# Performance work log

Hardware: AMD Instinct MI355X
Metric: run time of the kernel (lower is better)

## Reference

```python
import jax, jax.numpy as jnp
import numpy as np

H = 8
D_MODEL = 1024
D_K = D_MODEL // H
NEG = -1000000000.0


def layer_norm(x, a, b, eps=1e-06):
    # torch std: unbiased (ddof=1); module divides by (std + eps)
    mean = jnp.mean(x, axis=-1, keepdims=True)
    var = jnp.sum((x - mean) ** 2, axis=-1, keepdims=True) / (x.shape[-1] - 1)
    std = jnp.sqrt(var)
    return a * (x - mean) / (std + eps) + b


def setup_inputs() -> dict:
    key = jax.random.key(0)
    ks = jax.random.split(key, 12)
    B, S, D = 8, 1024, D_MODEL
    inp = {
        "query": jax.random.normal(ks[0], (B, S, D), jnp.float32),
        "value": jax.random.normal(ks[1], (B, S, D), jnp.float32),
        "key": jax.random.normal(ks[2], (B, S, D), jnp.float32),
        "mask": jax.random.randint(ks[3], (B, S), 0, 2, jnp.int32),
        "ln_a": jnp.ones((D,), jnp.float32),
        "ln_b": jnp.zeros((D,), jnp.float32),
        "wq": jax.random.normal(ks[4], (D, D), jnp.float32) * 0.02,
        "bq": jnp.zeros((D,), jnp.float32),
        "wk": jax.random.normal(ks[5], (D, D), jnp.float32) * 0.02,
        "bk": jnp.zeros((D,), jnp.float32),
        "wv": jax.random.normal(ks[6], (D, D), jnp.float32) * 0.02,
        "bv": jnp.zeros((D,), jnp.float32),
        "w_aoa": jax.random.normal(ks[7], (2 * D, 2 * D), jnp.float32) * 0.02,  # [out, in]
        "b_aoa": jnp.zeros((2 * D,), jnp.float32),
    }
    return inp


def reference(query, value, key, mask, ln_a, ln_b, wq, bq, wk, bk, wv, bv, w_aoa, b_aoa):
    B, S, D = query.shape
    # mask [B,S] -> [B,1,1,S]
    m = mask[:, None, None, :]
    # norm_q
    q = layer_norm(query, ln_a, ln_b)
    # QKV projections, split heads -> [B,H,S,Dk]
    def split_heads(x):
        return x.reshape(B, -1, H, D_K).transpose(0, 2, 1, 3)
    q_ = split_heads(q @ wq.T + bq)
    k_ = split_heads(key @ wk.T + bk)
    v_ = split_heads(value @ wv.T + bv)
    scores = jnp.einsum("bhqd,bhkd->bhqk", q_, k_) / jnp.sqrt(jnp.float32(D_K))
    scores = jnp.where(m == 0, NEG, scores)
    p = jax.nn.softmax(scores, axis=-1)
    x = jnp.einsum("bhqk,bhkd->bhqd", p, v_)
    x = x.transpose(0, 2, 1, 3).reshape(B, S, D)
    # AoA: concat with (normed) query, linear to 2D, GLU
    z = jnp.concatenate([x, q], axis=-1) @ w_aoa.T + b_aoa
    a, g = jnp.split(z, 2, axis=-1)
    return a * jax.nn.sigmoid(g)
```

## Files before the change

kernel.cpp:

```cpp
#include <hip/hip_runtime.h>

typedef __attribute__((ext_vector_type(8))) __bf16 bf16x8;
typedef __attribute__((ext_vector_type(4))) float f32x4;
typedef __attribute__((ext_vector_type(16))) float f32x16;

__device__ __forceinline__ ushort f2b(float f) {
    uint u = __builtin_bit_cast(uint, f);
    u += 0x7fffu + ((u >> 16) & 1u);
    return (ushort)(u >> 16);
}
__device__ __forceinline__ float b2f(ushort h) {
    uint u = ((uint)h) << 16;
    return __builtin_bit_cast(float, u);
}

__global__ __launch_bounds__(256) void cast_kernel(const float* __restrict__ src,
                                                   ushort* __restrict__ dst) {
    size_t i = ((size_t)blockIdx.x * 256 + threadIdx.x) * 4;
    float4 v = *(const float4*)(src + i);
    ushort4 o;
    o.x = f2b(v.x); o.y = f2b(v.y); o.z = f2b(v.z); o.w = f2b(v.w);
    *(ushort4*)(dst + i) = o;
}

__global__ __launch_bounds__(256) void cast_permute_aoa(const float* __restrict__ src,
                                                        ushort* __restrict__ dst) {
    int n1 = blockIdx.x >> 1;
    int c = (blockIdx.x & 1) * 1024 + threadIdx.x * 4;
    int q = ((n1 & 63) | ((n1 >> 7) << 6)) + ((n1 >> 6) & 1) * 1024;
    float4 v = *(const float4*)(src + (size_t)q * 2048 + c);
    ushort4 o;
    o.x = f2b(v.x); o.y = f2b(v.y); o.z = f2b(v.z); o.w = f2b(v.w);
    *(ushort4*)(dst + (size_t)n1 * 2048 + c) = o;
}

__global__ __launch_bounds__(256) void ln_kernel(const float* __restrict__ x,
                                                 const float* __restrict__ ga,
                                                 const float* __restrict__ be,
                                                 ushort* __restrict__ xq) {
    const int row = blockIdx.x, tid = threadIdx.x;
    __shared__ float red[4];
    float4 v = ((const float4*)(x + (size_t)row * 1024))[tid];
    float sm = v.x + v.y + v.z + v.w;
    for (int off = 32; off; off >>= 1) sm += __shfl_xor(sm, off);
    if ((tid & 63) == 0) red[tid >> 6] = sm;
    __syncthreads();
    float mean = (red[0] + red[1] + red[2] + red[3]) * (1.f / 1024.f);
    __syncthreads();
    float dx = v.x - mean, dy = v.y - mean, dz = v.z - mean, dw = v.w - mean;
    float s2 = dx * dx + dy * dy + dz * dz + dw * dw;
    for (int off = 32; off; off >>= 1) s2 += __shfl_xor(s2, off);
    if ((tid & 63) == 0) red[tid >> 6] = s2;
    __syncthreads();
    float var = (red[0] + red[1] + red[2] + red[3]) * (1.f / 1023.f);
    float inv = 1.f / (sqrtf(var) + 1e-6f);
    float4 g = ((const float4*)ga)[tid];
    float4 bb = ((const float4*)be)[tid];
    ushort4 o;
    o.x = f2b(g.x * dx * inv + bb.x);
    o.y = f2b(g.y * dy * inv + bb.y);
    o.z = f2b(g.z * dz * inv + bb.z);
    o.w = f2b(g.w * dw * inv + bb.w);
    *(ushort4*)&xq[(size_t)row * 2048 + 1024 + tid * 4] = o;
}

template <int MODE>
__global__ __launch_bounds__(512, 2) void gemm6(const ushort* __restrict__ Aq, int ldaq,
                                                const ushort* __restrict__ Ak,
                                                const ushort* __restrict__ Av,
                                                const ushort* __restrict__ B, int ldb,
                                                const float* __restrict__ bias0,
                                                const float* __restrict__ bias1,
                                                const float* __restrict__ bias2,
                                                void* __restrict__ out0,
                                                void* __restrict__ out1,
                                                void* __restrict__ out2,
                                                int K, int NB, float qscale) {
    __shared__ ushort lds[2][32768];

    const int tid = threadIdx.x;
    const int w = tid >> 6, l = tid & 63;
    const int wr = w >> 2, wcn = w & 3;
    const int r16 = l & 15, g4 = l >> 4;

    const int bid = blockIdx.x;
    const int cpx = gridDim.x >> 3;
    const int swz = (bid & 7) * cpx + (bid >> 3);
    const int m0 = (swz / NB) * 256;
    const int n0 = (swz % NB) * 256;

    const int region = (MODE == 0) ? (n0 >> 10) : 0;
    const ushort* A = (MODE == 0) ? (region == 0 ? Aq : (region == 1 ? Ak : Av)) : Aq;
    const int lda = (MODE == 0) ? (region == 0 ? ldaq : 1024) : ldaq;

    const int srow8 = l >> 3;
    const int sxor8 = ((l & 7) ^ srow8) * 8;
    const ushort* As0 = A + (size_t)(m0 + w * 8 + srow8) * lda + sxor8;
    const ushort* Bs0 = B + (size_t)(n0 + w * 8 + srow8) * ldb + sxor8;

    f32x4 acc[8][4];
#pragma unroll
    for (int i = 0; i < 8; i++)
#pragma unroll
        for (int j = 0; j < 4; j++) acc[i][j] = (f32x4){0.f, 0.f, 0.f, 0.f};

    const int sw16 = (r16 & 7) << 4;
    char* ldsb = (char*)&lds[0][0];

#define STAGE_H(sel_, HS_, kt_)                                                            \
    do {                                                                                   \
        const int mat_ = (HS_)&1, half_ = (HS_) >> 1;                                      \
        const ushort* sb_ = mat_ ? Bs0 : As0;                                              \
        const int ld_ = mat_ ? ldb : lda;                                                  \
        _Pragma("unroll") for (int li_ = 0; li_ < 2; li_++) {                              \
            const ushort* src_ = sb_ + (size_t)(half_ * 128 + li_ * 64) * ld_ + (kt_)*64;  \
            int dst_ = (sel_)*65536 + mat_ * 32768 + half_ * 16384 + li_ * 8192 + w * 1024;\
            __builtin_amdgcn_global_load_lds(                                              \
                (const __attribute__((address_space(1))) void*)src_,                       \
                (__attribute__((address_space(3))) void*)(ldsb + dst_), 16, 0, 0);         \
        }                                                                                  \
    } while (0)

    auto LDA4 = [&](bf16x8 (&dst)[4][2], int sel, int half) {
#pragma unroll
        for (int ai = 0; ai < 4; ai++)
#pragma unroll
            for (int ks = 0; ks < 2; ks++)
                dst[ai][ks] = *(const bf16x8*)(ldsb + sel * 65536 + half * 16384 +
                                               (wr * 16 + 32 * ai + r16) * 128 +
                                               ((ks * 64 + g4 * 16) ^ sw16));
    };
    auto LDB2 = [&](bf16x8 (&dst)[2][2], int sel, int half) {
#pragma unroll
        for (int bi = 0; bi < 2; bi++)
#pragma unroll
            for (int ks = 0; ks < 2; ks++)
                dst[bi][ks] = *(const bf16x8*)(ldsb + sel * 65536 + 32768 + half * 16384 +
                                               (wcn * 16 + 64 * bi + r16) * 128 +
                                               ((ks * 64 + g4 * 16) ^ sw16));
    };
    auto MM = [&](bf16x8 (&af)[4][2], bf16x8 (&bf)[2][2], int A0, int B0) {
        __builtin_amdgcn_s_setprio(1);
#pragma unroll
        for (int ks = 0; ks < 2; ks++)
#pragma unroll
            for (int ai = 0; ai < 4; ai++)
#pragma unroll
                for (int bi = 0; bi < 2; bi++)
                    acc[A0 + ai][B0 + bi] = __builtin_amdgcn_mfma_f32_16x16x32_bf16(
                        af[ai][ks], bf[bi][ks], acc[A0 + ai][B0 + bi], 0, 0, 0);
        __builtin_amdgcn_s_setprio(0);
    };

    const int NT = K >> 6;

    STAGE_H(0, 0, 0); STAGE_H(0, 1, 0); STAGE_H(0, 2, 0); STAGE_H(0, 3, 0);
    STAGE_H(1, 0, 1); STAGE_H(1, 1, 1); STAGE_H(1, 2, 1);
    asm volatile("s_waitcnt vmcnt(10)" ::: "memory");
    __builtin_amdgcn_s_barrier();

    bf16x8 aL[4][2], aH[4][2], bL[2][2], bH[2][2];

    for (int t = 0; t < NT - 2; ++t) {
        const int sel = t & 1;
        LDA4(aL, sel, 0); LDB2(bL, sel, 0);
        STAGE_H(sel ^ 1, 3, t + 1);
        __builtin_amdgcn_s_barrier();
        MM(aL, bL, 0, 0);
        asm volatile("s_waitcnt vmcnt(10)" ::: "memory");
        __builtin_amdgcn_s_barrier();
        LDA4(aH, sel, 1);
        STAGE_H(sel, 0, t + 2);
        __builtin_amdgcn_s_barrier();
        MM(aH, bL, 4, 0);
        asm volatile("s_waitcnt vmcnt(10)" ::: "memory");
        __builtin_amdgcn_s_barrier();
        LDB2(bH, sel, 1);
        STAGE_H(sel, 1, t + 2);
        __builtin_amdgcn_s_barrier();
        MM(aH, bH, 4, 2);
        __builtin_amdgcn_s_barrier();
        STAGE_H(sel, 2, t + 2);
        __builtin_amdgcn_s_barrier();
        MM(aL, bH, 0, 2);
        asm volatile("s_waitcnt vmcnt(10)" ::: "memory");
        __builtin_amdgcn_s_barrier();
    }
    {
        const int sel = (NT - 2) & 1;
        LDA4(aL, sel, 0); LDB2(bL, sel, 0);
        STAGE_H(sel ^ 1, 3, NT - 1);
        __builtin_amdgcn_s_barrier();
        MM(aL, bL, 0, 0);
        asm volatile("s_waitcnt vmcnt(10)" ::: "memory");
        __builtin_amdgcn_s_barrier();
        LDA4(aH, sel, 1);
        __builtin_amdgcn_s_barrier();
        MM(aH, bL, 4, 0);
        asm volatile("s_waitcnt vmcnt(8)" ::: "memory");
        __builtin_amdgcn_s_barrier();
        LDB2(bH, sel, 1);
        __builtin_amdgcn_s_barrier();
        MM(aH, bH, 4, 2);
        __builtin_amdgcn_s_barrier();
        MM(aL, bH, 0, 2);
        asm volatile("s_waitcnt vmcnt(4)" ::: "memory");
        __builtin_amdgcn_s_barrier();
    }
    {
        const int sel = (NT - 1) & 1;
        LDA4(aL, sel, 0); LDB2(bL, sel, 0);
        __builtin_amdgcn_s_barrier();
        MM(aL, bL, 0, 0);
        asm volatile("s_waitcnt vmcnt(2)" ::: "memory");
        __builtin_amdgcn_s_barrier();
        LDA4(aH, sel, 1);
        __builtin_amdgcn_s_barrier();
        MM(aH, bL, 4, 0);
        asm volatile("s_waitcnt vmcnt(0)" ::: "memory");
        __builtin_amdgcn_s_barrier();
        LDB2(bH, sel, 1);
        MM(aH, bH, 4, 2);
        MM(aL, bH, 0, 2);
    }
#undef STAGE_H

    if (MODE == 1) {
        float* out = (float*)out0;
#pragma unroll
        for (int bp = 0; bp < 2; bp++) {
            int j = (n0 >> 1) + wcn * 16 + 64 * bp + r16;
            float bsa = bias0[j];
            float bsg = bias0[j + 1024];
#pragma unroll
            for (int a_ = 0; a_ < 8; a_++) {
                int mr = m0 + wr * 16 + 32 * a_ + g4 * 4;
#pragma unroll
                for (int r = 0; r < 4; r++) {
                    float av = acc[a_][2 * bp][r] + bsa;
                    float gv = acc[a_][2 * bp + 1][r] + bsg;
                    out[(size_t)(mr + r) * 1024 + j] = av * (1.f / (1.f + __expf(-gv)));
                }
            }
        }
    } else {
        const int nr0 = n0 & 1023;
        const float* bias = region == 0 ? bias0 : (region == 1 ? bias1 : bias2);
        const float scale = region == 0 ? qscale : 1.f;
        if (region < 2) {
            ushort* C = (ushort*)(region == 0 ? out0 : out1);
#pragma unroll
            for (int b_ = 0; b_ < 4; b_++) {
                int n = nr0 + wcn * 16 + 64 * b_ + r16;
                float bs = bias[n];
#pragma unroll
                for (int a_ = 0; a_ < 8; a_++) {
                    int mr = m0 + wr * 16 + 32 * a_ + g4 * 4;
#pragma unroll
                    for (int r = 0; r < 4; r++)
                        C[(size_t)(mr + r) * 1024 + n] = f2b((acc[a_][b_][r] + bs) * scale);
                }
            }
        } else {
            ushort* Vt = (ushort*)out2;
#pragma unroll
            for (int b_ = 0; b_ < 4; b_++) {
                int n = nr0 + wcn * 16 + 64 * b_ + r16;
                float bs = bias[n];
                int h = n >> 7, d = n & 127;
#pragma unroll
                for (int a_ = 0; a_ < 8; a_++) {
                    int mr = m0 + wr * 16 + 32 * a_ + g4 * 4;
                    int bb = mr >> 10, s_ = mr & 1023;
                    ushort4 o;
                    o.x = f2b(acc[a_][b_][0] + bs);
                    o.y = f2b(acc[a_][b_][1] + bs);
                    o.z = f2b(acc[a_][b_][2] + bs);
                    o.w = f2b(acc[a_][b_][3] + bs);
                    *(ushort4*)&Vt[((size_t)(bb * 8 + h) * 128 + d) * 1024 + s_] = o;
                }
            }
        }
    }
}

__global__ __launch_bounds__(512, 2) void attn_kernel(const ushort* __restrict__ Q,
                                                      const ushort* __restrict__ Kt,
                                                      const ushort* __restrict__ Vt,
                                                      const int* __restrict__ mask,
                                                      ushort* __restrict__ xq) {
    __shared__ ushort Ks[2][8192];
    __shared__ ushort Vs[2][8192];
    __shared__ ushort Pl[8][2048];

    const int tid = threadIdx.x;
    const int l = tid & 63, wid = tid >> 6;
    const int ql = l & 31, hi = l >> 5;
    const int id = blockIdx.x;
    const int bh = ((id >> 5) << 3) | (id & 7);
    const int qb = (id >> 3) & 3;
    const int b = bh >> 3, h = bh & 7;
    const int q0 = qb * 256 + wid * 32;

    bf16x8 qf[8];
    const ushort* Qrow = Q + (size_t)(b * 1024 + q0 + ql) * 1024 + h * 128 + hi * 8;
#pragma unroll
    for (int ks = 0; ks < 8; ks++) qf[ks] = *(const bf16x8*)(Qrow + ks * 16);

    const ushort* Kg = Kt + ((size_t)b * 1024) * 1024 + h * 128;
    const ushort* Vg = Vt + (size_t)(b * 8 + h) * 128 * 1024;
    const int* mptr = mask + b * 1024;

    f32x16 xacc[4];
#pragma unroll
    for (int i = 0; i < 4; i++)
#pragma unroll
        for (int r = 0; r < 16; r++) xacc[i][r] = 0.f;
    float mrow = -INFINITY, lrow = 0.f, sclp = 0.f;

    char* Pme = (char*)&Pl[wid][0];
    const int pswz = (ql & 7) << 4;

    auto STAGE_K = [&](int sel, int t) {
        const int kv0 = t * 64;
#pragma unroll
        for (int it = 0; it < 2; ++it) {
            int ob = it * 8192 + wid * 1024;
            int o = ob + l * 16;
            int row = o >> 8;
            int sc = (o & 255) ^ ((row & 7) << 4);
            const ushort* src = Kg + (size_t)(kv0 + row) * 1024 + (sc >> 1);
            __builtin_amdgcn_global_load_lds((const __attribute__((address_space(1))) void*)src,
                (__attribute__((address_space(3))) void*)((char*)&Ks[sel][0] + ob), 16, 0, 0);
        }
    };
    auto STAGE_V = [&](int sel, int t) {
        const int kv0 = t * 64;
#pragma unroll
        for (int it = 0; it < 2; ++it) {
            int ob = it * 8192 + wid * 1024;
            int o = ob + l * 16;
            int d = o >> 7;
            int sc = (o & 127) ^ ((d & 7) << 4);
            const ushort* src = Vg + (size_t)d * 1024 + kv0 + (sc >> 1);
            __builtin_amdgcn_global_load_lds((const __attribute__((address_space(1))) void*)src,
                (__attribute__((address_space(3))) void*)((char*)&Vs[sel][0] + ob), 16, 0, 0);
        }
    };

    auto QK = [&](f32x16 (&s)[2], int sel, unsigned long long wt) {
        const char* Kb_ = (const char*)&Ks[sel][0];
#pragma unroll
        for (int sub = 0; sub < 2; sub++) {
            f32x16 sacc;
#pragma unroll
            for (int r = 0; r < 16; r++) sacc[r] = 0.f;
            const int rowk = sub * 32 + ql;
            const char* kr = Kb_ + rowk * 256;
            const int sw = (rowk & 7) << 4;
            __builtin_amdgcn_s_setprio(1);
#pragma unroll
            for (int ks = 0; ks < 8; ks++) {
                bf16x8 kfr = *(const bf16x8*)(kr + ((ks * 32 + hi * 16) ^ sw));
                sacc = __builtin_amdgcn_mfma_f32_32x32x16_bf16(kfr, qf[ks], sacc, 0, 0, 0);
            }
            __builtin_amdgcn_s_setprio(0);
#pragma unroll
            for (int q2 = 0; q2 < 4; q2++) {
                uint nib = (uint)(wt >> (8 * q2 + 4 * hi + 32 * sub)) & 15u;
#pragma unroll
                for (int r = 0; r < 4; r++)
                    if (!((nib >> r) & 1u)) sacc[4 * q2 + r] = -1e9f;
            }
            s[sub] = sacc;
        }
    };
    auto PV = [&](int sel) {
        const char* Vb_ = (const char*)&Vs[sel][0];
        const int vsw = (ql & 7) << 4;
#pragma unroll
        for (int df = 0; df < 4; df++)
#pragma unroll
            for (int r = 0; r < 16; r++) xacc[df][r] *= sclp;
#pragma unroll
        for (int ks2 = 0; ks2 < 4; ks2++) {
            bf16x8 pfr = *(const bf16x8*)(Pme + ql * 128 + ((ks2 * 32 + hi * 16) ^ pswz));
            __builtin_amdgcn_s_setprio(1);
#pragma unroll
            for (int df = 0; df < 4; df++) {
                const int d = df * 32 + ql;
                bf16x8 vfr = *(const bf16x8*)(Vb_ + d * 128 + ((ks2 * 32 + hi * 16) ^ vsw));
                xacc[df] = __builtin_amdgcn_mfma_f32_32x32x16_bf16(vfr, pfr, xacc[df], 0, 0, 0);
            }
            __builtin_amdgcn_s_setprio(0);
        }
    };
    auto SOFTMAX = [&](f32x16 (&s)[2]) {
        float pmax = -INFINITY;
#pragma unroll
        for (int res = 0; res < 2; res++)
#pragma unroll
            for (int r = 0; r < 16; r++) pmax = fmaxf(pmax, s[res][r]);
        pmax = fmaxf(pmax, __shfl_xor(pmax, 32));
        float mn = fmaxf(mrow, pmax);
        sclp = __expf(mrow - mn);
        mrow = mn;
        float rsum = 0.f;
#pragma unroll
        for (int res = 0; res < 2; res++)
#pragma unroll
            for (int r = 0; r < 16; r++) {
                float p = __expf(s[res][r] - mn);
                s[res][r] = p;
                rsum += p;
            }
        rsum += __shfl_xor(rsum, 32);
        lrow = lrow * sclp + rsum;
#pragma unroll
        for (int res = 0; res < 2; res++)
#pragma unroll
            for (int q2 = 0; q2 < 4; q2++) {
                uint lo = ((uint)f2b(s[res][4 * q2 + 1]) << 16) | f2b(s[res][4 * q2]);
                uint hi2 = ((uint)f2b(s[res][4 * q2 + 3]) << 16) | f2b(s[res][4 * q2 + 2]);
                uint2 pk; pk.x = lo; pk.y = hi2;
                *(uint2*)(Pme + ql * 128 + ((16 * q2 + 8 * hi + 64 * res) ^ pswz)) = pk;
            }
    };

    STAGE_K(0, 0);
    int mv = mptr[l];
    asm volatile("s_waitcnt vmcnt(0)" ::: "memory");
    __syncthreads();
    STAGE_K(1, 1);
    STAGE_V(0, 0);
    unsigned long long wt = __ballot(mv != 0);
    mv = mptr[64 + l];
    f32x16 s[2];
    QK(s, 0, wt);
    SOFTMAX(s);
    int kc = 1, vc = 0;

    for (int u = 1; u < 16; ++u) {
        wt = __ballot(mv != 0);
        asm volatile("s_waitcnt vmcnt(0)" ::: "memory");
        __syncthreads();
        if (u < 15) STAGE_K(kc ^ 1, u + 1);
        STAGE_V(vc ^ 1, u);
        if (u < 15) mv = mptr[(u + 1) * 64 + l];

        QK(s, kc, wt);
        PV(vc);
        SOFTMAX(s);

        kc ^= 1; vc ^= 1;
    }

    asm volatile("s_waitcnt vmcnt(0)" ::: "memory");
    __syncthreads();
    PV(vc);

    const float inv = 1.f / lrow;
    const size_t orow = (size_t)(b * 1024 + q0 + ql) * 2048 + h * 128;
#pragma unroll
    for (int df = 0; df < 4; df++) {
#pragma unroll
        for (int q2 = 0; q2 < 4; q2++) {
            ushort4 o;
            o.x = f2b(xacc[df][4 * q2 + 0] * inv);
            o.y = f2b(xacc[df][4 * q2 + 1] * inv);
            o.z = f2b(xacc[df][4 * q2 + 2] * inv);
            o.w = f2b(xacc[df][4 * q2 + 3] * inv);
            *(ushort4*)&xq[orow + df * 32 + 8 * q2 + 4 * hi] = o;
        }
    }
}

extern "C" void kernel_launch(void* const* d_in, const int* in_sizes, int n_in,
                              void* d_out, int out_size, void* d_ws, size_t ws_size,
                              hipStream_t stream) {
    const float* query = (const float*)d_in[0];
    const float* value = (const float*)d_in[1];
    const float* key   = (const float*)d_in[2];
    const int*   mask  = (const int*)d_in[3];
    const float* ln_a  = (const float*)d_in[4];
    const float* ln_b  = (const float*)d_in[5];
    const float* wq    = (const float*)d_in[6];
    const float* bq    = (const float*)d_in[7];
    const float* wk    = (const float*)d_in[8];
    const float* bk    = (const float*)d_in[9];
    const float* wv    = (const float*)d_in[10];
    const float* bv    = (const float*)d_in[11];
    const float* waoa  = (const float*)d_in[12];
    const float* baoa  = (const float*)d_in[13];
    float* out = (float*)d_out;

    char* w8 = (char*)d_ws;
    ushort* xq   = (ushort*)(w8);
    ushort* Qb   = (ushort*)(w8 + 33554432);
    ushort* Kb   = (ushort*)(w8 + 50331648);
    ushort* Vt   = (ushort*)(w8 + 67108864);
    ushort* keyb = (ushort*)(w8 + 83886080);
    ushort* valb = (ushort*)(w8 + 100663296);
    ushort* wqb  = (ushort*)(w8 + 117440512);
    ushort* wkb  = (ushort*)(w8 + 119537664);
    ushort* wvb  = (ushort*)(w8 + 121634816);
    ushort* wab  = (ushort*)(w8 + 123731968);

    cast_kernel<<<8192, 256, 0, stream>>>(key, keyb);
    cast_kernel<<<8192, 256, 0, stream>>>(value, valb);
    cast_kernel<<<1024, 256, 0, stream>>>(wq, wqb);
    cast_kernel<<<1024, 256, 0, stream>>>(wk, wkb);
    cast_kernel<<<1024, 256, 0, stream>>>(wv, wvb);
    cast_permute_aoa<<<4096, 256, 0, stream>>>(waoa, wab);
    ln_kernel<<<8192, 256, 0, stream>>>(query, ln_a, ln_b, xq);

    const float qscale = 0.08838834764831845f;

    gemm6<0><<<384, 512, 0, stream>>>(xq + 1024, 2048, keyb, valb,
                                      wqb, 1024, bq, bk, bv,
                                      Qb, Kb, Vt, 1024, 12, qscale);

    attn_kernel<<<256, 512, 0, stream>>>(Qb, Kb, Vt, mask, xq);

    gemm6<1><<<256, 512, 0, stream>>>(xq, 2048, nullptr, nullptr,
                                      wab, 2048, baoa, nullptr, nullptr,
                                      out, nullptr, nullptr, 2048, 8, 1.f);
}
```

Before: 239.5 us.

## Keep softmax probabilities in registers via permlane32 swap and shrink attention blocks

The P tile no longer round-trips through LDS. Probabilities are packed with v_cvt_pk_bf16_f32 and rearranged across half-waves with permlane32_swap so they can feed the PV MFMA directly as operands. The attention block shrinks from 8 waves to 4, with 512 blocks each handling 128 queries and the K/V staging loops adjusted to match. This saves LDS traffic and LDS space for P but doubles the K/V tile loads per query, since fewer waves share each staged tile.

```diff
diff --git a/kernel.cpp b/kernel.cpp
--- a/kernel.cpp
+++ b/kernel.cpp
@@ -3,6 +3,7 @@
 typedef __attribute__((ext_vector_type(8))) __bf16 bf16x8;
 typedef __attribute__((ext_vector_type(4))) float f32x4;
 typedef __attribute__((ext_vector_type(16))) float f32x16;
+typedef __attribute__((ext_vector_type(2))) int i32x2;
 
 __device__ __forceinline__ ushort f2b(float f) {
     uint u = __builtin_bit_cast(uint, f);
@@ -12,6 +13,11 @@
 __device__ __forceinline__ float b2f(ushort h) {
     uint u = ((uint)h) << 16;
     return __builtin_bit_cast(float, u);
+}
+__device__ __forceinline__ uint cvtpk(float a, float b) {
+    uint r;
+    asm("v_cvt_pk_bf16_f32 %0, %1, %2" : "=v"(r) : "v"(a), "v"(b));
+    return r;
 }
 
 __global__ __launch_bounds__(256) void cast_kernel(const float* __restrict__ src,
@@ -284,23 +290,22 @@
     }
 }
 
-__global__ __launch_bounds__(512, 2) void attn_kernel(const ushort* __restrict__ Q,
+__global__ __launch_bounds__(256, 2) void attn_kernel(const ushort* __restrict__ Q,
                                                       const ushort* __restrict__ Kt,
                                                       const ushort* __restrict__ Vt,
                                                       const int* __restrict__ mask,
                                                       ushort* __restrict__ xq) {
     __shared__ ushort Ks[2][8192];
     __shared__ ushort Vs[2][8192];
-    __shared__ ushort Pl[8][2048];
 
     const int tid = threadIdx.x;
     const int l = tid & 63, wid = tid >> 6;
     const int ql = l & 31, hi = l >> 5;
     const int id = blockIdx.x;
-    const int bh = ((id >> 5) << 3) | (id & 7);
-    const int qb = (id >> 3) & 3;
+    const int bh = ((id >> 6) << 3) | (id & 7);
+    const int qb = (id >> 3) & 7;
     const int b = bh >> 3, h = bh & 7;
-    const int q0 = qb * 256 + wid * 32;
+    const int q0 = qb * 128 + wid * 32;
 
     bf16x8 qf[8];
     const ushort* Qrow = Q + (size_t)(b * 1024 + q0 + ql) * 1024 + h * 128 + hi * 8;
@@ -317,15 +322,13 @@
 #pragma unroll
         for (int r = 0; r < 16; r++) xacc[i][r] = 0.f;
     float mrow = -INFINITY, lrow = 0.f, sclp = 0.f;
-
-    char* Pme = (char*)&Pl[wid][0];
-    const int pswz = (ql & 7) << 4;
+    bf16x8 pa[4];
 
     auto STAGE_K = [&](int sel, int t) {
         const int kv0 = t * 64;
 #pragma unroll
-        for (int it = 0; it < 2; ++it) {
-            int ob = it * 8192 + wid * 1024;
+        for (int it = 0; it < 4; ++it) {
+            int ob = it * 4096 + wid * 1024;
             int o = ob + l * 16;
             int row = o >> 8;
             int sc = (o & 255) ^ ((row & 7) << 4);
@@ -337,8 +340,8 @@
     auto STAGE_V = [&](int sel, int t) {
         const int kv0 = t * 64;
 #pragma unroll
-        for (int it = 0; it < 2; ++it) {
-            int ob = it * 8192 + wid * 1024;
+        for (int it = 0; it < 4; ++it) {
+            int ob = it * 4096 + wid * 1024;
             int o = ob + l * 16;
             int d = o >> 7;
             int sc = (o & 127) ^ ((d & 7) << 4);
@@ -377,23 +380,21 @@
     };
     auto PV = [&](int sel) {
         const char* Vb_ = (const char*)&Vs[sel][0];
-        const int vsw = (ql & 7) << 4;
 #pragma unroll
         for (int df = 0; df < 4; df++)
 #pragma unroll
             for (int r = 0; r < 16; r++) xacc[df][r] *= sclp;
+        __builtin_amdgcn_s_setprio(1);
 #pragma unroll
         for (int ks2 = 0; ks2 < 4; ks2++) {
-            bf16x8 pfr = *(const bf16x8*)(Pme + ql * 128 + ((ks2 * 32 + hi * 16) ^ pswz));
-            __builtin_amdgcn_s_setprio(1);
 #pragma unroll
             for (int df = 0; df < 4; df++) {
                 const int d = df * 32 + ql;
-                bf16x8 vfr = *(const bf16x8*)(Vb_ + d * 128 + ((ks2 * 32 + hi * 16) ^ vsw));
-                xacc[df] = __builtin_amdgcn_mfma_f32_32x32x16_bf16(vfr, pfr, xacc[df], 0, 0, 0);
-            }
-            __builtin_amdgcn_s_setprio(0);
-        }
+                bf16x8 vfr = *(const bf16x8*)(Vb_ + d * 128 + ((ks2 * 32 + hi * 16) ^ ((d & 7) << 4)));
+                xacc[df] = __builtin_amdgcn_mfma_f32_32x32x16_bf16(vfr, pa[ks2], xacc[df], 0, 0, 0);
+            }
+        }
+        __builtin_amdgcn_s_setprio(0);
     };
     auto SOFTMAX = [&](f32x16 (&s)[2]) {
         float pmax = -INFINITY;
@@ -417,13 +418,22 @@
         rsum += __shfl_xor(rsum, 32);
         lrow = lrow * sclp + rsum;
 #pragma unroll
-        for (int res = 0; res < 2; res++)
-#pragma unroll
-            for (int q2 = 0; q2 < 4; q2++) {
-                uint lo = ((uint)f2b(s[res][4 * q2 + 1]) << 16) | f2b(s[res][4 * q2]);
-                uint hi2 = ((uint)f2b(s[res][4 * q2 + 3]) << 16) | f2b(s[res][4 * q2 + 2]);
-                uint2 pk; pk.x = lo; pk.y = hi2;
-                *(uint2*)(Pme + ql * 128 + ((16 * q2 + 8 * hi + 64 * res) ^ pswz)) = pk;
+        for (int sub = 0; sub < 2; sub++)
+#pragma unroll
+            for (int g = 0; g < 2; g++) {
+                const int b0 = g * 8;
+                uint lo01 = cvtpk(s[sub][b0 + 0], s[sub][b0 + 1]);
+                uint lo23 = cvtpk(s[sub][b0 + 2], s[sub][b0 + 3]);
+                uint hi01 = cvtpk(s[sub][b0 + 4], s[sub][b0 + 5]);
+                uint hi23 = cvtpk(s[sub][b0 + 6], s[sub][b0 + 7]);
+                i32x2 r02 = __builtin_amdgcn_permlane32_swap((int)lo01, (int)hi01, false, false);
+                i32x2 r13 = __builtin_amdgcn_permlane32_swap((int)lo23, (int)hi23, false, false);
+                union { bf16x8 v; uint u[4]; } pk;
+                pk.u[0] = (uint)r02.x;
+                pk.u[1] = (uint)r13.x;
+                pk.u[2] = (uint)r02.y;
+                pk.u[3] = (uint)r13.y;
+                pa[sub * 2 + g] = pk.v;
             }
     };
 
@@ -520,7 +530,7 @@
                                       wqb, 1024, bq, bk, bv,
                                       Qb, Kb, Vt, 1024, 12, qscale);
 
-    attn_kernel<<<256, 512, 0, stream>>>(Qb, Kb, Vt, mask, xq);
+    attn_kernel<<<512, 256, 0, stream>>>(Qb, Kb, Vt, mask, xq);
 
     gemm6<1><<<256, 512, 0, stream>>>(xq, 2048, nullptr, nullptr,
                                       wab, 2048, baoa, nullptr, nullptr,
```

Result: faster. 232.2 us (-3.0%).
